# Performance work log

Hardware: AMD Instinct MI355X
Metric: run time of the kernel (lower is better)

## Reference

```python
import jax, jax.numpy as jnp
import numpy as np

N, E, F_IN, H, C = 50000, 800000, 128, 4, 64
NEG_SLOPE = 0.2
LN_EPS = 1e-5


def setup_inputs() -> dict:
    key = jax.random.key(0)
    ks = jax.random.split(key, 8)
    s = 0.05
    return {
        "x": jax.random.normal(ks[0], (N, F_IN), jnp.float32),
        "edge_index": jax.random.randint(ks[1], (2, E), 0, N, jnp.int64).astype(jnp.int32),
        "Wl": jax.random.normal(ks[2], (F_IN, H * C), jnp.float32) * s,
        "bl": jnp.zeros((H * C,), jnp.float32),
        "Wr": jax.random.normal(ks[3], (F_IN, H * C), jnp.float32) * s,
        "br": jnp.zeros((H * C,), jnp.float32),
        "att": jax.random.normal(ks[4], (H, C), jnp.float32) * s,
        "bias_out": jnp.zeros((H * C,), jnp.float32),
        "Wproj": jax.random.normal(ks[5], (H * C, C), jnp.float32) * s,
        "ln_w": jnp.ones((C,), jnp.float32),
        "ln_b": jnp.zeros((C,), jnp.float32),
        "Wres": jax.random.normal(ks[6], (F_IN, C), jnp.float32) * s,
    }


def reference(x, edge_index, Wl, bl, Wr, br, att, bias_out, Wproj, ln_w, ln_b, Wres):
    n = x.shape[0]
    # add self loops (GATv2Conv add_self_loops=True)
    loop = jnp.arange(n, dtype=edge_index.dtype)
    src = jnp.concatenate([edge_index[0], loop])
    dst = jnp.concatenate([edge_index[1], loop])

    xl = (x @ Wl + bl).reshape(n, H, C)  # source-side transform
    xr = (x @ Wr + br).reshape(n, H, C)  # target-side transform

    # GATv2 edge scores: a^T LeakyReLU(xl_j + xr_i)
    m = xl[src] + xr[dst]                              # [Etot, H, C]
    e = jnp.einsum('ehc,hc->eh', jax.nn.leaky_relu(m, NEG_SLOPE), att)

    # segment softmax over incoming edges per destination node
    emax = jax.ops.segment_max(e, dst, num_segments=n)  # every node has a self loop
    ex = jnp.exp(e - emax[dst])
    denom = jax.ops.segment_sum(ex, dst, num_segments=n)
    alpha = ex / denom[dst]                             # [Etot, H]

    # scatter-aggregate messages, concat heads, output bias
    msg = xl[src] * alpha[:, :, None]                   # [Etot, H, C]
    out = jax.ops.segment_sum(msg, dst, num_segments=n).reshape(n, H * C) + bias_out

    # proj -> layernorm -> GELU -> (+ residual); dropout inactive in eval
    out = out @ Wproj                                   # [N, C]
    mu = out.mean(-1, keepdims=True)
    var = jnp.mean(jnp.square(out - mu), -1, keepdims=True)
    out = (out - mu) * jax.lax.rsqrt(var + LN_EPS) * ln_w + ln_b
    out = jax.nn.gelu(out, approximate=False)
    return out + x @ Wres
```

## Files before the change

kernel.cpp:

```cpp
#include <hip/hip_runtime.h>
#include <math.h>

#define NEG_SLOPE 0.2f
#define LN_EPS 1e-5f
#define HC 256
#define NHEAD 4
#define CDIM 64
#define FIN 128
#define CAP 96
#define CCAP 256

typedef short bf16x8 __attribute__((ext_vector_type(8)));
typedef float f32x4  __attribute__((ext_vector_type(4)));

__device__ inline unsigned short f2bf(float f) {
    unsigned u = __builtin_bit_cast(unsigned, f);
    return (unsigned short)((u + 0x7FFFu + ((u >> 16) & 1u)) >> 16);
}
__device__ inline float bf2f(unsigned short s) {
    return __builtin_bit_cast(float, (unsigned)s << 16);
}
__device__ inline void unpack8(const uint4 u, float* f) {
    f[0] = __builtin_bit_cast(float, u.x << 16);
    f[1] = __builtin_bit_cast(float, u.x & 0xffff0000u);
    f[2] = __builtin_bit_cast(float, u.y << 16);
    f[3] = __builtin_bit_cast(float, u.y & 0xffff0000u);
    f[4] = __builtin_bit_cast(float, u.z << 16);
    f[5] = __builtin_bit_cast(float, u.z & 0xffff0000u);
    f[6] = __builtin_bit_cast(float, u.w << 16);
    f[7] = __builtin_bit_cast(float, u.w & 0xffff0000u);
}

__global__ __launch_bounds__(256) void k_prep(
    const float* __restrict__ Wl, const float* __restrict__ Wr,
    const float* __restrict__ Wproj, const float* __restrict__ Wres,
    const float* __restrict__ bias_out, const float* __restrict__ att,
    ushort* __restrict__ wlb, ushort* __restrict__ wrb,
    ushort* __restrict__ wpj, ushort* __restrict__ wrs,
    float* __restrict__ bpj, float* __restrict__ att_s)
{
    const int t = threadIdx.x;
    const int b = blockIdx.x;
    if (b < 224) {
        const int gid = b * 256 + t;
        if (gid < 32768) {
            const int idx = gid;
            const int j = idx & 7, n = (idx >> 3) & 255, q = idx >> 11;
            const int k = (q >> 2) * 32 + (q & 3) * 8 + j;
            wlb[idx] = f2bf(Wl[k * HC + n]);
            wrb[idx] = f2bf(Wr[k * HC + n]);
        } else if (gid < 49152) {
            const int idx = gid - 32768;
            const int j = idx & 7, n = (idx >> 3) & 63, q = idx >> 9;
            const int k = (q >> 2) * 32 + (q & 3) * 8 + j;
            wpj[idx] = f2bf(Wproj[k * CDIM + n]);
        } else {
            const int idx = gid - 49152;
            const int j = idx & 7, n = (idx >> 3) & 63, q = idx >> 9;
            const int k = (q >> 2) * 32 + (q & 3) * 8 + j;
            wrs[idx] = f2bf(Wres[k * CDIM + n]);
        }
    } else {
        att_s[t] = att[t] * 1.44269504088896f;
        __shared__ float part[4][CDIM];
        const int col = t & 63, q = t >> 6;
        float s = 0.f;
        for (int k = q * 64; k < q * 64 + 64; ++k)
            s += bias_out[k] * Wproj[k * CDIM + col];
        part[q][col] = s;
        __syncthreads();
        if (q == 0)
            bpj[col] = part[0][col] + part[1][col] + part[2][col] + part[3][col];
    }
}

__global__ __launch_bounds__(256) void k_scatterA(
    const int* __restrict__ ei, int* __restrict__ ccnt, int2* __restrict__ cbkt,
    int E)
{
    const int gid = blockIdx.x * 256 + threadIdx.x;
    if (gid < E) {
        const int s = ei[gid];
        const int d = ei[E + gid];
        const int cb = d >> 3;
        const int slot = atomicAdd(&ccnt[cb], 1);
        cbkt[(size_t)cb * CCAP + slot] = make_int2(d, s);
    }
}

__global__ __launch_bounds__(256) void k_scatterB(
    const int* __restrict__ ccnt, const int2* __restrict__ cbkt,
    int* __restrict__ cnt, int* __restrict__ bucket, int n_nodes)
{
    __shared__ int lcnt[8];
    const int t = threadIdx.x;
    const int b = blockIdx.x;
    if (t < 8) lcnt[t] = 0;
    __syncthreads();
    const int n = min(ccnt[b], CCAP);
    for (int i = t; i < n; i += 256) {
        const int2 p = cbkt[(size_t)b * CCAP + i];
        const int slot = atomicAdd(&lcnt[p.x & 7], 1);
        bucket[p.x * CAP + slot] = p.y;
    }
    __syncthreads();
    if (t < 8) {
        const int d = b * 8 + t;
        if (d < n_nodes) cnt[d] = lcnt[t];
    }
}

__global__ __launch_bounds__(256) void k_linear_mfma(
    const float* __restrict__ x,
    const ushort* __restrict__ wlb, const ushort* __restrict__ wrb,
    const float* __restrict__ bl, const float* __restrict__ br,
    ushort* __restrict__ x_bf,
    ushort* __restrict__ xl, ushort* __restrict__ xr, int n_nodes)
{
    const int wid = blockIdx.x * 4 + (threadIdx.x >> 6);
    const int lane = threadIdx.x & 63;
    const int ntiles = n_nodes >> 4;
    if (wid >= ntiles * 2) return;
    const int side = wid & 1;
    const int tile = wid >> 1;

    const ushort* __restrict__ wb   = side ? wrb : wlb;
    const float*  __restrict__ bias = side ? br : bl;
    ushort*       __restrict__ outp = side ? xr : xl;

    const int m  = lane & 15;
    const int kb = lane >> 4;
    const long arow = ((long)tile * 16 + m) * FIN;

    f32x4 acc[16];
#pragma unroll
    for (int f = 0; f < 16; ++f) acc[f] = (f32x4){0.f, 0.f, 0.f, 0.f};

    for (int ks = 0; ks < 4; ++ks) {
        const float4 lo = *reinterpret_cast<const float4*>(&x[arow + ks * 32 + kb * 8]);
        const float4 hi = *reinterpret_cast<const float4*>(&x[arow + ks * 32 + kb * 8 + 4]);
        union { bf16x8 v; ushort u[8]; } xf;
        xf.u[0] = f2bf(lo.x); xf.u[1] = f2bf(lo.y);
        xf.u[2] = f2bf(lo.z); xf.u[3] = f2bf(lo.w);
        xf.u[4] = f2bf(hi.x); xf.u[5] = f2bf(hi.y);
        xf.u[6] = f2bf(hi.z); xf.u[7] = f2bf(hi.w);
        if (side == 0)
            *reinterpret_cast<bf16x8*>(&x_bf[arow + ks * 32 + kb * 8]) = xf.v;

        const ushort* __restrict__ wq = wb + (size_t)((ks * 4 + kb) * HC) * 8;
#pragma unroll
        for (int f = 0; f < 16; ++f) {
            const bf16x8 wf = *reinterpret_cast<const bf16x8*>(&wq[(f * 16 + m) * 8]);
            acc[f] = __builtin_amdgcn_mfma_f32_16x16x32_bf16(wf, xf.v, acc[f], 0, 0, 0);
        }
    }
    const long obase = ((long)tile * 16 + m) * HC;
#pragma unroll
    for (int f = 0; f < 16; ++f) {
        const int ch = f * 16 + kb * 4;
        const float4 bi = *reinterpret_cast<const float4*>(&bias[ch]);
        ushort4 o;
        o.x = f2bf(acc[f][0] + bi.x);
        o.y = f2bf(acc[f][1] + bi.y);
        o.z = f2bf(acc[f][2] + bi.z);
        o.w = f2bf(acc[f][3] + bi.w);
        *reinterpret_cast<ushort4*>(&outp[obase + ch]) = o;
    }
}

__global__ __launch_bounds__(256) void k_gat_gather(
    const int* __restrict__ cnt, const int* __restrict__ bucket,
    const ushort* __restrict__ xl, const ushort* __restrict__ xr,
    const float* __restrict__ att_s,
    ushort* __restrict__ agg, int n_nodes)
{
    const int node = blockIdx.x * 4 + (threadIdx.x >> 6);
    const int lane = threadIdx.x & 63;
    if (node >= n_nodes) return;

    const int cn = cnt[node];
    const int half = lane >> 5;
    const unsigned ch = (unsigned)(lane & 31) * 8;

    float xrv[8], atv[8];
    unpack8(*reinterpret_cast<const uint4*>(&xr[(unsigned)node * HC + ch]), xrv);
    const float4 a0 = *reinterpret_cast<const float4*>(&att_s[ch]);
    const float4 a1 = *reinterpret_cast<const float4*>(&att_s[ch + 4]);
    atv[0] = a0.x; atv[1] = a0.y; atv[2] = a0.z; atv[3] = a0.w;
    atv[4] = a1.x; atv[5] = a1.y; atv[6] = a1.z; atv[7] = a1.w;

    float cs[8];
    unpack8(*reinterpret_cast<const uint4*>(&xl[(unsigned)node * HC + ch]), cs);
    float ps = 0.f;
#pragma unroll
    for (int j = 0; j < 8; ++j) {
        float m = cs[j] + xrv[j];
        m = fmaxf(m, NEG_SLOPE * m);
        ps += m * atv[j];
    }
    ps += __shfl_xor(ps, 1);
    ps += __shfl_xor(ps, 2);
    ps += __shfl_xor(ps, 4);
    float es;
    asm("v_exp_f32 %0, %1" : "=v"(es) : "v"(ps));
    es = (half == 0) ? es : 0.f;
    float den = es;
    float ac[8];
#pragma unroll
    for (int j = 0; j < 8; ++j) ac[j] = es * cs[j];

    if (cn > 0) {
        const int beg = node * CAP;
        const int end = beg + cn;
        const int last = end - 1;

        const int i0 = bucket[min(beg + half, last)];
        const int i1 = bucket[min(beg + 2 + half, last)];
        const int i2 = bucket[min(beg + 4 + half, last)];
        const int i3 = bucket[min(beg + 6 + half, last)];
        int ip = bucket[min(beg + 8 + half, last)];
        int iq = bucket[min(beg + 10 + half, last)];
        uint4 d0 = *reinterpret_cast<const uint4*>(&xl[((unsigned)i0 << 8) + ch]);
        uint4 d1 = *reinterpret_cast<const uint4*>(&xl[((unsigned)i1 << 8) + ch]);
        uint4 d2 = *reinterpret_cast<const uint4*>(&xl[((unsigned)i2 << 8) + ch]);
        uint4 d3 = *reinterpret_cast<const uint4*>(&xl[((unsigned)i3 << 8) + ch]);

        for (int k = beg; k < end; k += 2) {
            const uint4 cu = d0;
            d0 = d1; d1 = d2; d2 = d3;
            d3 = *reinterpret_cast<const uint4*>(&xl[((unsigned)ip << 8) + ch]);
            ip = iq;
            iq = bucket[min(k + 12 + half, last)];

            float c[8];
            unpack8(cu, c);
            float p = 0.f;
#pragma unroll
            for (int j = 0; j < 8; ++j) {
                float m = c[j] + xrv[j];
                m = fmaxf(m, NEG_SLOPE * m);
                p += m * atv[j];
            }
            p += __shfl_xor(p, 1);
            p += __shfl_xor(p, 2);
            p += __shfl_xor(p, 4);

            float e;
            asm("v_exp_f32 %0, %1" : "=v"(e) : "v"(p));
            e = (k + half < end) ? e : 0.f;
            den += e;
#pragma unroll
            for (int j = 0; j < 8; ++j) ac[j] += e * c[j];
        }
    }

    den += __shfl_xor(den, 32);
#pragma unroll
    for (int j = 0; j < 8; ++j) ac[j] += __shfl_xor(ac[j], 32);

    if (lane < 32) {
        const float inv = 1.f / den;
        uint4 o;
        o.x = ((unsigned)f2bf(ac[1] * inv) << 16) | f2bf(ac[0] * inv);
        o.y = ((unsigned)f2bf(ac[3] * inv) << 16) | f2bf(ac[2] * inv);
        o.z = ((unsigned)f2bf(ac[5] * inv) << 16) | f2bf(ac[4] * inv);
        o.w = ((unsigned)f2bf(ac[7] * inv) << 16) | f2bf(ac[6] * inv);
        *reinterpret_cast<uint4*>(&agg[(unsigned)node * HC + ch]) = o;
    }
}

__global__ __launch_bounds__(256) void k_post_mfma(
    const ushort* __restrict__ aggb, const ushort* __restrict__ xb,
    const ushort* __restrict__ wpj, const ushort* __restrict__ wrs,
    const float* __restrict__ bpj,
    const float* __restrict__ ln_w, const float* __restrict__ ln_b,
    float* __restrict__ out, int n_nodes)
{
    const int wid = blockIdx.x * 4 + (threadIdx.x >> 6);
    const int lane = threadIdx.x & 63;
    const int ntiles = n_nodes >> 4;
    if (wid >= ntiles) return;

    const int m  = lane & 15;
    const int kb = lane >> 4;
    const long node = (long)wid * 16 + m;
    const long gbase = node * HC;
    const long xbase = node * FIN;

    f32x4 ap[4], ar[4];
#pragma unroll
    for (int f = 0; f < 4; ++f) {
        ap[f] = (f32x4){0.f, 0.f, 0.f, 0.f};
        ar[f] = (f32x4){0.f, 0.f, 0.f, 0.f};
    }

    for (int ks = 0; ks < 8; ++ks) {
        const bf16x8 af = *reinterpret_cast<const bf16x8*>(&aggb[gbase + ks * 32 + kb * 8]);
        const ushort* __restrict__ wq = wpj + (size_t)((ks * 4 + kb) * CDIM) * 8;
#pragma unroll
        for (int f = 0; f < 4; ++f) {
            const bf16x8 wf = *reinterpret_cast<const bf16x8*>(&wq[(f * 16 + m) * 8]);
            ap[f] = __builtin_amdgcn_mfma_f32_16x16x32_bf16(wf, af, ap[f], 0, 0, 0);
        }
    }
    for (int ks = 0; ks < 4; ++ks) {
        const bf16x8 af = *reinterpret_cast<const bf16x8*>(&xb[xbase + ks * 32 + kb * 8]);
        const ushort* __restrict__ wq = wrs + (size_t)((ks * 4 + kb) * CDIM) * 8;
#pragma unroll
        for (int f = 0; f < 4; ++f) {
            const bf16x8 wf = *reinterpret_cast<const bf16x8*>(&wq[(f * 16 + m) * 8]);
            ar[f] = __builtin_amdgcn_mfma_f32_16x16x32_bf16(wf, af, ar[f], 0, 0, 0);
        }
    }

    float p[4][4];
#pragma unroll
    for (int f = 0; f < 4; ++f) {
        const float4 bp = *reinterpret_cast<const float4*>(&bpj[f * 16 + kb * 4]);
#pragma unroll
        for (int j = 0; j < 4; ++j) p[f][j] = ap[f][j] + ((const float*)&bp)[j];
    }

    float s1 = 0.f;
#pragma unroll
    for (int f = 0; f < 4; ++f)
#pragma unroll
        for (int j = 0; j < 4; ++j) s1 += p[f][j];
    s1 += __shfl_xor(s1, 16); s1 += __shfl_xor(s1, 32);
    const float mu = s1 * (1.f / 64.f);

    float s2 = 0.f;
#pragma unroll
    for (int f = 0; f < 4; ++f)
#pragma unroll
        for (int j = 0; j < 4; ++j) {
            const float d = p[f][j] - mu;
            s2 += d * d;
        }
    s2 += __shfl_xor(s2, 16); s2 += __shfl_xor(s2, 32);
    const float rs = rsqrtf(s2 * (1.f / 64.f) + LN_EPS);

#pragma unroll
    for (int f = 0; f < 4; ++f) {
        const int ch = f * 16 + kb * 4;
        const float4 lw = *reinterpret_cast<const float4*>(&ln_w[ch]);
        const float4 lb = *reinterpret_cast<const float4*>(&ln_b[ch]);
        float4 ov;
#pragma unroll
        for (int j = 0; j < 4; ++j) {
            const float v = (p[f][j] - mu) * rs * ((const float*)&lw)[j] + ((const float*)&lb)[j];
            const float g = 0.5f * v * (1.f + erff(v * 0.70710678118654752f));
            ((float*)&ov)[j] = g + ar[f][j];
        }
        *reinterpret_cast<float4*>(&out[node * CDIM + ch]) = ov;
    }
}

extern "C" void kernel_launch(void* const* d_in, const int* in_sizes, int n_in,
                              void* d_out, int out_size, void* d_ws, size_t ws_size,
                              hipStream_t stream)
{
    const float* x        = (const float*)d_in[0];
    const int*   ei       = (const int*)  d_in[1];
    const float* Wl       = (const float*)d_in[2];
    const float* bl       = (const float*)d_in[3];
    const float* Wr       = (const float*)d_in[4];
    const float* br       = (const float*)d_in[5];
    const float* att      = (const float*)d_in[6];
    const float* bias_out = (const float*)d_in[7];
    const float* Wproj    = (const float*)d_in[8];
    const float* ln_w     = (const float*)d_in[9];
    const float* ln_b     = (const float*)d_in[10];
    const float* Wres     = (const float*)d_in[11];
    float* out = (float*)d_out;

    const int N = in_sizes[0] / FIN;
    const int E = in_sizes[1] / 2;
    const int ntiles = N >> 4;
    const int NCB = (N + 7) >> 3;

    ushort* us = (ushort*)d_ws;
    size_t uo = 0;
    ushort* xl_bf  = us + uo; uo += (size_t)N * HC;
    ushort* xr_bf  = us + uo; uo += (size_t)N * HC;
    ushort* agg_bf = us + uo; uo += (size_t)N * HC;
    ushort* x_bf   = us + uo; uo += (size_t)N * FIN;
    ushort* wlb    = us + uo; uo += 32768;
    ushort* wrb    = us + uo; uo += 32768;
    ushort* wpj    = us + uo; uo += 16384;
    ushort* wrs    = us + uo; uo += 8192;
    float* bpj   = (float*)(us + uo);
    float* att_s = bpj + CDIM;
    int* cnt    = (int*)(att_s + HC);
    int* ccnt   = cnt + N;
    int* bucket = ccnt + NCB;
    int2* cbkt  = (int2*)(bucket + (size_t)N * CAP);

    hipMemsetAsync(ccnt, 0, (size_t)NCB * sizeof(int), stream);

    k_prep<<<225, 256, 0, stream>>>(Wl, Wr, Wproj, Wres, bias_out, att,
                                    wlb, wrb, wpj, wrs, bpj, att_s);

    k_scatterA<<<(E + 255) / 256, 256, 0, stream>>>(ei, ccnt, cbkt, E);
    k_scatterB<<<NCB, 256, 0, stream>>>(ccnt, cbkt, cnt, bucket, N);

    k_linear_mfma<<<(2 * ntiles + 3) / 4, 256, 0, stream>>>(
        x, wlb, wrb, bl, br, x_bf, xl_bf, xr_bf, N);

    k_gat_gather<<<(N + 3) / 4, 256, 0, stream>>>(
        cnt, bucket, xl_bf, xr_bf, att_s, agg_bf, N);

    k_post_mfma<<<(ntiles + 3) / 4, 256, 0, stream>>>(
        agg_bf, x_bf, wpj, wrs, bpj, ln_w, ln_b, out, N);
}
```

Measured before the change: 212.2 us.

## Fuse launches: prep with scatterA, scatterB with linear, gather with post-MLP

Merges the six kernels into three. Weight prep and the edge bucketing pass share one launch, as do the per-node bucket finalisation and the linear MFMA. The GAT gather is fused with the projection, LayerNorm and GELU stage, so each 16-node tile keeps its aggregated rows in LDS instead of writing agg to global memory and reading it back. The fused stage now splits the 64 output channels across the 4 waves and computes LayerNorm statistics with a cross-wave shared-memory reduction using E[x^2]-mu^2. This removes launch gaps and the agg round trip, at the cost of less parallel gather (one block per 16 nodes, 4 nodes serialized per wave) and a block barrier.

```diff
diff --git a/kernel.cpp b/kernel.cpp
--- a/kernel.cpp
+++ b/kernel.cpp
@@ -31,13 +31,15 @@
     f[7] = __builtin_bit_cast(float, u.w & 0xffff0000u);
 }
 
-__global__ __launch_bounds__(256) void k_prep(
+__global__ __launch_bounds__(256) void k_prep_scA(
     const float* __restrict__ Wl, const float* __restrict__ Wr,
     const float* __restrict__ Wproj, const float* __restrict__ Wres,
     const float* __restrict__ bias_out, const float* __restrict__ att,
+    const int* __restrict__ ei,
     ushort* __restrict__ wlb, ushort* __restrict__ wrb,
     ushort* __restrict__ wpj, ushort* __restrict__ wrs,
-    float* __restrict__ bpj, float* __restrict__ att_s)
+    float* __restrict__ bpj, float* __restrict__ att_s,
+    int* __restrict__ ccnt, int2* __restrict__ cbkt, int E)
 {
     const int t = threadIdx.x;
     const int b = blockIdx.x;
@@ -60,7 +62,7 @@
             const int k = (q >> 2) * 32 + (q & 3) * 8 + j;
             wrs[idx] = f2bf(Wres[k * CDIM + n]);
         }
-    } else {
+    } else if (b == 224) {
         att_s[t] = att[t] * 1.44269504088896f;
         __shared__ float part[4][CDIM];
         const int col = t & 63, q = t >> 6;
@@ -71,54 +73,49 @@
         __syncthreads();
         if (q == 0)
             bpj[col] = part[0][col] + part[1][col] + part[2][col] + part[3][col];
-    }
-}
-
-__global__ __launch_bounds__(256) void k_scatterA(
-    const int* __restrict__ ei, int* __restrict__ ccnt, int2* __restrict__ cbkt,
-    int E)
-{
-    const int gid = blockIdx.x * 256 + threadIdx.x;
-    if (gid < E) {
-        const int s = ei[gid];
-        const int d = ei[E + gid];
-        const int cb = d >> 3;
-        const int slot = atomicAdd(&ccnt[cb], 1);
-        cbkt[(size_t)cb * CCAP + slot] = make_int2(d, s);
-    }
-}
-
-__global__ __launch_bounds__(256) void k_scatterB(
+    } else {
+        const int gid = (b - 225) * 256 + t;
+        if (gid < E) {
+            const int s = ei[gid];
+            const int d = ei[E + gid];
+            const int cb = d >> 3;
+            const int slot = atomicAdd(&ccnt[cb], 1);
+            cbkt[(size_t)cb * CCAP + slot] = make_int2(d, s);
+        }
+    }
+}
+
+__global__ __launch_bounds__(256) void k_scB_linear(
     const int* __restrict__ ccnt, const int2* __restrict__ cbkt,
-    int* __restrict__ cnt, int* __restrict__ bucket, int n_nodes)
-{
-    __shared__ int lcnt[8];
-    const int t = threadIdx.x;
-    const int b = blockIdx.x;
-    if (t < 8) lcnt[t] = 0;
-    __syncthreads();
-    const int n = min(ccnt[b], CCAP);
-    for (int i = t; i < n; i += 256) {
-        const int2 p = cbkt[(size_t)b * CCAP + i];
-        const int slot = atomicAdd(&lcnt[p.x & 7], 1);
-        bucket[p.x * CAP + slot] = p.y;
-    }
-    __syncthreads();
-    if (t < 8) {
-        const int d = b * 8 + t;
-        if (d < n_nodes) cnt[d] = lcnt[t];
-    }
-}
-
-__global__ __launch_bounds__(256) void k_linear_mfma(
+    int* __restrict__ cnt, int* __restrict__ bucket,
     const float* __restrict__ x,
     const ushort* __restrict__ wlb, const ushort* __restrict__ wrb,
     const float* __restrict__ bl, const float* __restrict__ br,
     ushort* __restrict__ x_bf,
-    ushort* __restrict__ xl, ushort* __restrict__ xr, int n_nodes)
+    ushort* __restrict__ xl, ushort* __restrict__ xr,
+    int nb_scb, int E, int n_nodes)
 {
-    const int wid = blockIdx.x * 4 + (threadIdx.x >> 6);
-    const int lane = threadIdx.x & 63;
+    const int t = threadIdx.x;
+    if (blockIdx.x < nb_scb) {
+        __shared__ int lcnt[8];
+        const int b = blockIdx.x;
+        if (t < 8) lcnt[t] = 0;
+        __syncthreads();
+        const int n = min(ccnt[b], CCAP);
+        for (int i = t; i < n; i += 256) {
+            const int2 p = cbkt[(size_t)b * CCAP + i];
+            const int slot = atomicAdd(&lcnt[p.x & 7], 1);
+            bucket[p.x * CAP + slot] = p.y;
+        }
+        __syncthreads();
+        if (t < 8) {
+            const int d = b * 8 + t;
+            if (d < n_nodes) cnt[d] = lcnt[t];
+        }
+        return;
+    }
+    const int wid = (blockIdx.x - nb_scb) * 4 + (t >> 6);
+    const int lane = t & 63;
     const int ntiles = n_nodes >> 4;
     if (wid >= ntiles * 2) return;
     const int side = wid & 1;
@@ -168,191 +165,175 @@
     }
 }
 
-__global__ __launch_bounds__(256) void k_gat_gather(
+__global__ __launch_bounds__(256) void k_gat_post(
     const int* __restrict__ cnt, const int* __restrict__ bucket,
     const ushort* __restrict__ xl, const ushort* __restrict__ xr,
     const float* __restrict__ att_s,
-    ushort* __restrict__ agg, int n_nodes)
-{
-    const int node = blockIdx.x * 4 + (threadIdx.x >> 6);
-    const int lane = threadIdx.x & 63;
-    if (node >= n_nodes) return;
-
-    const int cn = cnt[node];
-    const int half = lane >> 5;
-    const unsigned ch = (unsigned)(lane & 31) * 8;
-
-    float xrv[8], atv[8];
-    unpack8(*reinterpret_cast<const uint4*>(&xr[(unsigned)node * HC + ch]), xrv);
-    const float4 a0 = *reinterpret_cast<const float4*>(&att_s[ch]);
-    const float4 a1 = *reinterpret_cast<const float4*>(&att_s[ch + 4]);
-    atv[0] = a0.x; atv[1] = a0.y; atv[2] = a0.z; atv[3] = a0.w;
-    atv[4] = a1.x; atv[5] = a1.y; atv[6] = a1.z; atv[7] = a1.w;
-
-    float cs[8];
-    unpack8(*reinterpret_cast<const uint4*>(&xl[(unsigned)node * HC + ch]), cs);
-    float ps = 0.f;
-#pragma unroll
-    for (int j = 0; j < 8; ++j) {
-        float m = cs[j] + xrv[j];
-        m = fmaxf(m, NEG_SLOPE * m);
-        ps += m * atv[j];
-    }
-    ps += __shfl_xor(ps, 1);
-    ps += __shfl_xor(ps, 2);
-    ps += __shfl_xor(ps, 4);
-    float es;
-    asm("v_exp_f32 %0, %1" : "=v"(es) : "v"(ps));
-    es = (half == 0) ? es : 0.f;
-    float den = es;
-    float ac[8];
-#pragma unroll
-    for (int j = 0; j < 8; ++j) ac[j] = es * cs[j];
-
-    if (cn > 0) {
-        const int beg = node * CAP;
-        const int end = beg + cn;
-        const int last = end - 1;
-
-        const int i0 = bucket[min(beg + half, last)];
-        const int i1 = bucket[min(beg + 2 + half, last)];
-        const int i2 = bucket[min(beg + 4 + half, last)];
-        const int i3 = bucket[min(beg + 6 + half, last)];
-        int ip = bucket[min(beg + 8 + half, last)];
-        int iq = bucket[min(beg + 10 + half, last)];
-        uint4 d0 = *reinterpret_cast<const uint4*>(&xl[((unsigned)i0 << 8) + ch]);
-        uint4 d1 = *reinterpret_cast<const uint4*>(&xl[((unsigned)i1 << 8) + ch]);
-        uint4 d2 = *reinterpret_cast<const uint4*>(&xl[((unsigned)i2 << 8) + ch]);
-        uint4 d3 = *reinterpret_cast<const uint4*>(&xl[((unsigned)i3 << 8) + ch]);
-
-        for (int k = beg; k < end; k += 2) {
-            const uint4 cu = d0;
-            d0 = d1; d1 = d2; d2 = d3;
-            d3 = *reinterpret_cast<const uint4*>(&xl[((unsigned)ip << 8) + ch]);
-            ip = iq;
-            iq = bucket[min(k + 12 + half, last)];
-
-            float c[8];
-            unpack8(cu, c);
-            float p = 0.f;
-#pragma unroll
-            for (int j = 0; j < 8; ++j) {
-                float m = c[j] + xrv[j];
-                m = fmaxf(m, NEG_SLOPE * m);
-                p += m * atv[j];
-            }
-            p += __shfl_xor(p, 1);
-            p += __shfl_xor(p, 2);
-            p += __shfl_xor(p, 4);
-
-            float e;
-            asm("v_exp_f32 %0, %1" : "=v"(e) : "v"(p));
-            e = (k + half < end) ? e : 0.f;
-            den += e;
-#pragma unroll
-            for (int j = 0; j < 8; ++j) ac[j] += e * c[j];
-        }
-    }
-
-    den += __shfl_xor(den, 32);
-#pragma unroll
-    for (int j = 0; j < 8; ++j) ac[j] += __shfl_xor(ac[j], 32);
-
-    if (lane < 32) {
-        const float inv = 1.f / den;
-        uint4 o;
-        o.x = ((unsigned)f2bf(ac[1] * inv) << 16) | f2bf(ac[0] * inv);
-        o.y = ((unsigned)f2bf(ac[3] * inv) << 16) | f2bf(ac[2] * inv);
-        o.z = ((unsigned)f2bf(ac[5] * inv) << 16) | f2bf(ac[4] * inv);
-        o.w = ((unsigned)f2bf(ac[7] * inv) << 16) | f2bf(ac[6] * inv);
-        *reinterpret_cast<uint4*>(&agg[(unsigned)node * HC + ch]) = o;
-    }
-}
-
-__global__ __launch_bounds__(256) void k_post_mfma(
-    const ushort* __restrict__ aggb, const ushort* __restrict__ xb,
+    const ushort* __restrict__ xb,
     const ushort* __restrict__ wpj, const ushort* __restrict__ wrs,
     const float* __restrict__ bpj,
     const float* __restrict__ ln_w, const float* __restrict__ ln_b,
     float* __restrict__ out, int n_nodes)
 {
-    const int wid = blockIdx.x * 4 + (threadIdx.x >> 6);
+    __shared__ uint4 lagg[16 * 32];
+    __shared__ float red1[4][16], red2[4][16];
+
+    const int tile = blockIdx.x;
+    const int w = threadIdx.x >> 6;
     const int lane = threadIdx.x & 63;
-    const int ntiles = n_nodes >> 4;
-    if (wid >= ntiles) return;
+    const int half = lane >> 5;
+    const unsigned ch = (unsigned)(lane & 31) * 8;
+
+    const float4 a0 = *reinterpret_cast<const float4*>(&att_s[ch]);
+    const float4 a1 = *reinterpret_cast<const float4*>(&att_s[ch + 4]);
+    float atv[8];
+    atv[0] = a0.x; atv[1] = a0.y; atv[2] = a0.z; atv[3] = a0.w;
+    atv[4] = a1.x; atv[5] = a1.y; atv[6] = a1.z; atv[7] = a1.w;
+
+#pragma unroll 1
+    for (int i = 0; i < 4; ++i) {
+        const int row = w * 4 + i;
+        const int node = tile * 16 + row;
+        if (node < n_nodes) {
+            float xrv[8], cs[8];
+            unpack8(*reinterpret_cast<const uint4*>(&xr[(unsigned)node * HC + ch]), xrv);
+            unpack8(*reinterpret_cast<const uint4*>(&xl[(unsigned)node * HC + ch]), cs);
+
+            float ps = 0.f;
+#pragma unroll
+            for (int j = 0; j < 8; ++j) {
+                float m = cs[j] + xrv[j];
+                m = fmaxf(m, NEG_SLOPE * m);
+                ps += m * atv[j];
+            }
+            ps += __shfl_xor(ps, 1);
+            ps += __shfl_xor(ps, 2);
+            ps += __shfl_xor(ps, 4);
+            float es;
+            asm("v_exp_f32 %0, %1" : "=v"(es) : "v"(ps));
+            es = (half == 0) ? es : 0.f;
+            float den = es;
+            float ac[8];
+#pragma unroll
+            for (int j = 0; j < 8; ++j) ac[j] = es * cs[j];
+
+            const int cn = cnt[node];
+            if (cn > 0) {
+                const int beg = node * CAP;
+                const int end = beg + cn;
+                const int last = end - 1;
+
+                const int i0 = bucket[min(beg + half, last)];
+                const int i1 = bucket[min(beg + 2 + half, last)];
+                const int i2 = bucket[min(beg + 4 + half, last)];
+                const int i3 = bucket[min(beg + 6 + half, last)];
+                int ip = bucket[min(beg + 8 + half, last)];
+                int iq = bucket[min(beg + 10 + half, last)];
+                uint4 d0 = *reinterpret_cast<const uint4*>(&xl[((unsigned)i0 << 8) + ch]);
+                uint4 d1 = *reinterpret_cast<const uint4*>(&xl[((unsigned)i1 << 8) + ch]);
+                uint4 d2 = *reinterpret_cast<const uint4*>(&xl[((unsigned)i2 << 8) + ch]);
+                uint4 d3 = *reinterpret_cast<const uint4*>(&xl[((unsigned)i3 << 8) + ch]);
+
+                for (int k = beg; k < end; k += 2) {
+                    const uint4 cu = d0;
+                    d0 = d1; d1 = d2; d2 = d3;
+                    d3 = *reinterpret_cast<const uint4*>(&xl[((unsigned)ip << 8) + ch]);
+                    ip = iq;
+                    iq = bucket[min(k + 12 + half, last)];
+
+                    float c[8];
+                    unpack8(cu, c);
+                    float p = 0.f;
+#pragma unroll
+                    for (int j = 0; j < 8; ++j) {
+                        float m = c[j] + xrv[j];
+                        m = fmaxf(m, NEG_SLOPE * m);
+                        p += m * atv[j];
+                    }
+                    p += __shfl_xor(p, 1);
+                    p += __shfl_xor(p, 2);
+                    p += __shfl_xor(p, 4);
+
+                    float e;
+                    asm("v_exp_f32 %0, %1" : "=v"(e) : "v"(p));
+                    e = (k + half < end) ? e : 0.f;
+                    den += e;
+#pragma unroll
+                    for (int j = 0; j < 8; ++j) ac[j] += e * c[j];
+                }
+            }
+
+            den += __shfl_xor(den, 32);
+#pragma unroll
+            for (int j = 0; j < 8; ++j) ac[j] += __shfl_xor(ac[j], 32);
+
+            if (lane < 32) {
+                const float inv = 1.f / den;
+                uint4 o;
+                o.x = ((unsigned)f2bf(ac[1] * inv) << 16) | f2bf(ac[0] * inv);
+                o.y = ((unsigned)f2bf(ac[3] * inv) << 16) | f2bf(ac[2] * inv);
+                o.z = ((unsigned)f2bf(ac[5] * inv) << 16) | f2bf(ac[4] * inv);
+                o.w = ((unsigned)f2bf(ac[7] * inv) << 16) | f2bf(ac[6] * inv);
+                lagg[row * 32 + ((lane & 31) ^ (row & 7))] = o;
+            }
+        }
+    }
+    __syncthreads();
 
     const int m  = lane & 15;
     const int kb = lane >> 4;
-    const long node = (long)wid * 16 + m;
-    const long gbase = node * HC;
+    const long node = (long)tile * 16 + m;
+
+    f32x4 ap = (f32x4){0.f, 0.f, 0.f, 0.f};
+    f32x4 ar = (f32x4){0.f, 0.f, 0.f, 0.f};
+
+#pragma unroll
+    for (int ks = 0; ks < 8; ++ks) {
+        const uint4 au = lagg[m * 32 + (((ks << 2) | kb) ^ (m & 7))];
+        const bf16x8 af = __builtin_bit_cast(bf16x8, au);
+        const bf16x8 wf = *reinterpret_cast<const bf16x8*>(
+            &wpj[(size_t)((ks * 4 + kb) * CDIM + w * 16 + m) * 8]);
+        ap = __builtin_amdgcn_mfma_f32_16x16x32_bf16(wf, af, ap, 0, 0, 0);
+    }
     const long xbase = node * FIN;
-
-    f32x4 ap[4], ar[4];
-#pragma unroll
-    for (int f = 0; f < 4; ++f) {
-        ap[f] = (f32x4){0.f, 0.f, 0.f, 0.f};
-        ar[f] = (f32x4){0.f, 0.f, 0.f, 0.f};
-    }
-
-    for (int ks = 0; ks < 8; ++ks) {
-        const bf16x8 af = *reinterpret_cast<const bf16x8*>(&aggb[gbase + ks * 32 + kb * 8]);
-        const ushort* __restrict__ wq = wpj + (size_t)((ks * 4 + kb) * CDIM) * 8;
-#pragma unroll
-        for (int f = 0; f < 4; ++f) {
-            const bf16x8 wf = *reinterpret_cast<const bf16x8*>(&wq[(f * 16 + m) * 8]);
-            ap[f] = __builtin_amdgcn_mfma_f32_16x16x32_bf16(wf, af, ap[f], 0, 0, 0);
-        }
-    }
+#pragma unroll
     for (int ks = 0; ks < 4; ++ks) {
         const bf16x8 af = *reinterpret_cast<const bf16x8*>(&xb[xbase + ks * 32 + kb * 8]);
-        const ushort* __restrict__ wq = wrs + (size_t)((ks * 4 + kb) * CDIM) * 8;
-#pragma unroll
-        for (int f = 0; f < 4; ++f) {
-            const bf16x8 wf = *reinterpret_cast<const bf16x8*>(&wq[(f * 16 + m) * 8]);
-            ar[f] = __builtin_amdgcn_mfma_f32_16x16x32_bf16(wf, af, ar[f], 0, 0, 0);
-        }
-    }
-
-    float p[4][4];
-#pragma unroll
-    for (int f = 0; f < 4; ++f) {
-        const float4 bp = *reinterpret_cast<const float4*>(&bpj[f * 16 + kb * 4]);
-#pragma unroll
-        for (int j = 0; j < 4; ++j) p[f][j] = ap[f][j] + ((const float*)&bp)[j];
-    }
-
-    float s1 = 0.f;
-#pragma unroll
-    for (int f = 0; f < 4; ++f)
-#pragma unroll
-        for (int j = 0; j < 4; ++j) s1 += p[f][j];
+        const bf16x8 wf = *reinterpret_cast<const bf16x8*>(
+            &wrs[(size_t)((ks * 4 + kb) * CDIM + w * 16 + m) * 8]);
+        ar = __builtin_amdgcn_mfma_f32_16x16x32_bf16(wf, af, ar, 0, 0, 0);
+    }
+
+    const float4 bp = *reinterpret_cast<const float4*>(&bpj[w * 16 + kb * 4]);
+    float p[4];
+    p[0] = ap[0] + bp.x; p[1] = ap[1] + bp.y;
+    p[2] = ap[2] + bp.z; p[3] = ap[3] + bp.w;
+
+    float s1 = p[0] + p[1] + p[2] + p[3];
+    float s2 = p[0] * p[0] + p[1] * p[1] + p[2] * p[2] + p[3] * p[3];
     s1 += __shfl_xor(s1, 16); s1 += __shfl_xor(s1, 32);
-    const float mu = s1 * (1.f / 64.f);
-
-    float s2 = 0.f;
-#pragma unroll
-    for (int f = 0; f < 4; ++f)
+    s2 += __shfl_xor(s2, 16); s2 += __shfl_xor(s2, 32);
+    if (lane < 16) { red1[w][m] = s1; red2[w][m] = s2; }
+    __syncthreads();
+
+    const float S1 = red1[0][m] + red1[1][m] + red1[2][m] + red1[3][m];
+    const float S2 = red2[0][m] + red2[1][m] + red2[2][m] + red2[3][m];
+    const float mu = S1 * (1.f / 64.f);
+    const float var = fmaxf(S2 * (1.f / 64.f) - mu * mu, 0.f);
+    const float rs = rsqrtf(var + LN_EPS);
+
+    if (node < n_nodes) {
+        const int cho = w * 16 + kb * 4;
+        const float4 lw = *reinterpret_cast<const float4*>(&ln_w[cho]);
+        const float4 lb = *reinterpret_cast<const float4*>(&ln_b[cho]);
+        float4 ov;
 #pragma unroll
         for (int j = 0; j < 4; ++j) {
-            const float d = p[f][j] - mu;
-            s2 += d * d;
-        }
-    s2 += __shfl_xor(s2, 16); s2 += __shfl_xor(s2, 32);
-    const float rs = rsqrtf(s2 * (1.f / 64.f) + LN_EPS);
-
-#pragma unroll
-    for (int f = 0; f < 4; ++f) {
-        const int ch = f * 16 + kb * 4;
-        const float4 lw = *reinterpret_cast<const float4*>(&ln_w[ch]);
-        const float4 lb = *reinterpret_cast<const float4*>(&ln_b[ch]);
-        float4 ov;
-#pragma unroll
-        for (int j = 0; j < 4; ++j) {
-            const float v = (p[f][j] - mu) * rs * ((const float*)&lw)[j] + ((const float*)&lb)[j];
+            const float v = (p[j] - mu) * rs * ((const float*)&lw)[j] + ((const float*)&lb)[j];
             const float g = 0.5f * v * (1.f + erff(v * 0.70710678118654752f));
-            ((float*)&ov)[j] = g + ar[f][j];
-        }
-        *reinterpret_cast<float4*>(&out[node * CDIM + ch]) = ov;
+            ((float*)&ov)[j] = g + ar[j];
+        }
+        *reinterpret_cast<float4*>(&out[node * CDIM + cho]) = ov;
     }
 }
 
@@ -383,7 +364,6 @@
     size_t uo = 0;
     ushort* xl_bf  = us + uo; uo += (size_t)N * HC;
     ushort* xr_bf  = us + uo; uo += (size_t)N * HC;
-    ushort* agg_bf = us + uo; uo += (size_t)N * HC;
     ushort* x_bf   = us + uo; uo += (size_t)N * FIN;
     ushort* wlb    = us + uo; uo += 32768;
     ushort* wrb    = us + uo; uo += 32768;
@@ -398,18 +378,21 @@
 
     hipMemsetAsync(ccnt, 0, (size_t)NCB * sizeof(int), stream);
 
-    k_prep<<<225, 256, 0, stream>>>(Wl, Wr, Wproj, Wres, bias_out, att,
-                                    wlb, wrb, wpj, wrs, bpj, att_s);
-
-    k_scatterA<<<(E + 255) / 256, 256, 0, stream>>>(ei, ccnt, cbkt, E);
-    k_scatterB<<<NCB, 256, 0, stream>>>(ccnt, cbkt, cnt, bucket, N);
-
-    k_linear_mfma<<<(2 * ntiles + 3) / 4, 256, 0, stream>>>(
-        x, wlb, wrb, bl, br, x_bf, xl_bf, xr_bf, N);
-
-    k_gat_gather<<<(N + 3) / 4, 256, 0, stream>>>(
-        cnt, bucket, xl_bf, xr_bf, att_s, agg_bf, N);
-
-    k_post_mfma<<<(ntiles + 3) / 4, 256, 0, stream>>>(
-        agg_bf, x_bf, wpj, wrs, bpj, ln_w, ln_b, out, N);
-}
+    {
+        const int nb_scA = (E + 255) / 256;
+        k_prep_scA<<<225 + nb_scA, 256, 0, stream>>>(
+            Wl, Wr, Wproj, Wres, bias_out, att, ei,
+            wlb, wrb, wpj, wrs, bpj, att_s, ccnt, cbkt, E);
+    }
+
+    {
+        const int nb_lin = (2 * ntiles + 3) / 4;
+        k_scB_linear<<<NCB + nb_lin, 256, 0, stream>>>(
+            ccnt, cbkt, cnt, bucket, x, wlb, wrb, bl, br,
+            x_bf, xl_bf, xr_bf, NCB, E, N);
+    }
+
+    k_gat_post<<<ntiles, 256, 0, stream>>>(
+        cnt, bucket, xl_bf, xr_bf, att_s, x_bf,
+        wpj, wrs, bpj, ln_w, ln_b, out, N);
+}
```

After: 230.0 us. +8.4%, slower.
